# Performance work log

Hardware: AMD Instinct MI355X
Metric: run time of the kernel (lower is better)

The kernel has to match this reference:

```python
import jax, jax.numpy as jnp
import numpy as np

N, F, S, D = 8, 16, 196, 1024
H = 8
HD = D // H
L = 1 + F * S  # global feature token + f*s patch tokens


def _ln(x, g, b, eps=1e-5):
    m = x.mean(-1, keepdims=True)
    v = ((x - m) ** 2).mean(-1, keepdims=True)
    return (x - m) / jnp.sqrt(v + eps) * g + b


def _attn(q, k, v, hd):
    s = jnp.einsum('bqd,bkd->bqk', q, k) / jnp.sqrt(jnp.asarray(hd, q.dtype))
    return jnp.einsum('bqk,bkd->bqd', jax.nn.softmax(s, axis=-1), v)


def setup_inputs() -> dict:
    key = jax.random.key(0)
    ks = jax.random.split(key, 8)
    sc = 0.02
    return {
        'x': jax.random.normal(ks[0], (N, L, D), jnp.float32),
        'W_in': jax.random.normal(ks[1], (D, D), jnp.float32) * sc,
        'b_in': jnp.zeros((D,), jnp.float32),
        'g_in': jnp.ones((D,), jnp.float32),
        'beta_in': jnp.zeros((D,), jnp.float32),
        'W_q': jax.random.normal(ks[2], (D, D), jnp.float32) * sc,
        'W_k': jax.random.normal(ks[3], (D, D), jnp.float32) * sc,
        'W_v': jax.random.normal(ks[4], (D, D), jnp.float32) * sc,
        'g_out': jnp.ones((D,), jnp.float32),
        'beta_out': jnp.zeros((D,), jnp.float32),
        'W_out': jax.random.normal(ks[5], (D, D), jnp.float32) * sc,
        'b_out': jnp.zeros((D,), jnp.float32),
        'att_type': 1,  # 1 == 'time', 0 == 'space' (static)
    }


def reference(x, W_in, b_in, g_in, beta_in, W_q, W_k, W_v, g_out, beta_out, W_out, b_out, att_type):
    n = x.shape[0]
    nh = n * H
    # in_fc: Linear + LayerNorm
    x = _ln(x @ W_in + b_in, g_in, beta_in)
    q, k, v = x @ W_q, x @ W_k, x @ W_v

    def split_heads(y):  # [n, L, D] -> [n*h, L, hd]
        return y.reshape(n, L, H, HD).transpose(0, 2, 1, 3).reshape(nh, L, HD)

    q, k, v = map(split_heads, (q, k, v))
    feat_q, q = q[:, :1], q[:, 1:]
    feat_k, k = k[:, :1], k[:, 1:]
    feat_v, v = v[:, :1], v[:, 1:]

    # token_att is computed in the original but never used (dead code):
    # token_att = _attn(feat_q, k, v, HD)

    if att_type == 1:  # time attention: windows of length F per spatial site
        qt = q.reshape(nh, F, S, HD).transpose(0, 2, 1, 3).reshape(nh * S, F, HD)
        kt = k.reshape(nh, F, S, HD).transpose(0, 2, 1, 3).reshape(nh * S, F, HD)
        vt = v.reshape(nh, F, S, HD).transpose(0, 2, 1, 3).reshape(nh * S, F, HD)
        fk = jnp.tile(feat_k, (S, 1, 1))  # torch .repeat(s,1,1)
        fv = jnp.tile(feat_v, (S, 1, 1))
        kk = jnp.concatenate((fk, kt), axis=1)  # [nh*s, 1+f, hd]
        vv = jnp.concatenate((fv, vt), axis=1)
        seq = _attn(qt, kk, vv, HD)  # [nh*s, f, hd]
        seq = seq.reshape(nh, S, F, HD).transpose(0, 2, 1, 3).reshape(nh, F * S, HD)
    else:  # space attention: windows of length S per frame
        qs = q.reshape(nh * F, S, HD)
        ks_ = k.reshape(nh * F, S, HD)
        vs = v.reshape(nh * F, S, HD)
        fk = jnp.tile(feat_k, (F, 1, 1))
        fv = jnp.tile(feat_v, (F, 1, 1))
        kk = jnp.concatenate((fk, ks_), axis=1)  # [nh*f, 1+s, hd]
        vv = jnp.concatenate((fv, vs), axis=1)
        seq = _attn(qs, kk, vv, HD)  # [nh*f, s, hd]
        seq = seq.reshape(nh, F * S, HD)

    out = jnp.concatenate((feat_q, seq), axis=1)  # [nh, L, hd]
    out = out.reshape(n, H, L, HD).transpose(0, 2, 1, 3).reshape(n, L, D)
    out = _ln(out, g_out, beta_out) @ W_out + b_out
    return out
```

## Files before the change

kernel.cpp:

```cpp
#include <hip/hip_runtime.h>
#include <stdint.h>

#define N_B 8
#define F_T 16
#define S_T 196
#define D_M 1024
#define H_N 8
#define HD  128
#define L_T 3137
#define M_R (N_B * L_T)
#define M_P 25216

typedef __attribute__((ext_vector_type(8))) short bf16x8;
typedef __attribute__((ext_vector_type(4))) float f32x4;

__device__ __forceinline__ float b2f(unsigned int u) {
  union { unsigned int i; float f; } x; x.i = u << 16; return x.f;
}
__device__ __forceinline__ unsigned short f2b(float f) {
  union { float f; unsigned int i; } x; x.f = f;
  unsigned int r = x.i + 0x7fffu + ((x.i >> 16) & 1u);
  return (unsigned short)(r >> 16);
}

__global__ __launch_bounds__(256) void convert_pad(const float* __restrict__ x,
                                                   unsigned short* __restrict__ xb,
                                                   int nreal) {
  int i = (blockIdx.x * 256 + threadIdx.x) * 4;
  float4 v;
  if (i < nreal) v = *(const float4*)(x + i);
  else { v.x = 0.f; v.y = 0.f; v.z = 0.f; v.w = 0.f; }
  ushort4 o;
  o.x = f2b(v.x); o.y = f2b(v.y); o.z = f2b(v.z); o.w = f2b(v.w);
  *(ushort4*)(xb + i) = o;
}

struct WP { const float* s[5]; unsigned short* d[5]; };
__global__ __launch_bounds__(256) void transpose5(WP p) {
  __shared__ float t[32][33];
  const int w = blockIdx.z;
  const float* W = p.s[w];
  unsigned short* Wt = p.d[w];
  const int tx = threadIdx.x, ty = threadIdx.y;
  const int n0 = blockIdx.x * 32, k0 = blockIdx.y * 32;
#pragma unroll
  for (int i = 0; i < 4; i++)
    t[ty + i * 8][tx] = W[(size_t)(k0 + ty + i * 8) * D_M + n0 + tx];
  __syncthreads();
#pragma unroll
  for (int i = 0; i < 4; i++)
    Wt[(size_t)(n0 + ty + i * 8) * D_M + k0 + tx] = f2b(t[tx][ty + i * 8]);
}

__device__ __forceinline__ void async16(const unsigned short* g, unsigned short* l) {
  __builtin_amdgcn_global_load_lds((const __attribute__((address_space(1))) void*)g,
                                   (__attribute__((address_space(3))) void*)l, 16, 0, 0);
}

struct Outs { void* p[3]; };

template <int MODE>
__global__ __launch_bounds__(256) void gemm_bt(const unsigned short* __restrict__ A,
                                               const unsigned short* __restrict__ Bt,
                                               const float* __restrict__ bias,
                                               Outs o, int Mreal) {
  constexpr int NCB = (MODE == 3) ? 24 : 8;
  __shared__ __align__(16) unsigned short lds[17408];
  unsigned short* As = lds;
  unsigned short* Bs = lds + 8192;
  const int tid = threadIdx.x;
  const int lane = tid & 63;
  const int wv = tid >> 6;
  const int wm = wv >> 1, wn = wv & 1;

  const int flat = blockIdx.y * NCB + blockIdx.x;
  int rowBase, colBase;
  if (MODE == 3) {
    const int lin = (flat & 7) * 591 + (flat >> 3);
    const int cg = lin / 1576;
    const int rem = lin - cg * 1576;
    rowBase = (rem >> 3) * 128;
    colBase = (cg * 8 + (rem & 7)) * 128;
  } else {
    const int lin = (flat & 7) * 197 + (flat >> 3);
    rowBase = (lin >> 3) * 128;
    colBase = (lin & 7) * 128;
  }

  const int srow8 = lane >> 3;
  const int gk = ((lane & 7) ^ srow8) * 8;
  const unsigned short* gA = A + (size_t)(rowBase + wv * 32 + srow8) * 1024 + gk;
  const unsigned short* gB = Bt + (size_t)(colBase + wv * 32 + srow8) * 1024 + gk;
  unsigned short* lA = As + wv * 2048 + lane * 8;
  unsigned short* lB = Bs + wv * 2048 + lane * 8;

  f32x4 acc[4][4] = {};

  const int mf = lane & 15, kg = lane >> 4;
  const int sl0 = ((kg) ^ (mf & 7)) * 8;
  const int sl1 = ((4 + kg) ^ (mf & 7)) * 8;
  const unsigned short* Ar = As + (wm * 64 + mf) * 64;
  const unsigned short* Br = Bs + (wn * 64 + mf) * 64;

  for (int kt = 0; kt < 1024; kt += 64) {
    __syncthreads();
#pragma unroll
    for (int ii = 0; ii < 4; ii++) {
      async16(gA + ii * 8 * 1024 + kt, lA + ii * 512);
      async16(gB + ii * 8 * 1024 + kt, lB + ii * 512);
    }
    __syncthreads();
    {
      bf16x8 av[4], bv[4];
#pragma unroll
      for (int i = 0; i < 4; i++) av[i] = *(const bf16x8*)(Ar + i * 1024 + sl0);
#pragma unroll
      for (int j = 0; j < 4; j++) bv[j] = *(const bf16x8*)(Br + j * 1024 + sl0);
#pragma unroll
      for (int i = 0; i < 4; i++)
#pragma unroll
        for (int j = 0; j < 4; j++)
          acc[i][j] = __builtin_amdgcn_mfma_f32_16x16x32_bf16(av[i], bv[j], acc[i][j], 0, 0, 0);
    }
    {
      bf16x8 av[4], bv[4];
#pragma unroll
      for (int i = 0; i < 4; i++) av[i] = *(const bf16x8*)(Ar + i * 1024 + sl1);
#pragma unroll
      for (int j = 0; j < 4; j++) bv[j] = *(const bf16x8*)(Br + j * 1024 + sl1);
#pragma unroll
      for (int i = 0; i < 4; i++)
#pragma unroll
        for (int j = 0; j < 4; j++)
          acc[i][j] = __builtin_amdgcn_mfma_f32_16x16x32_bf16(av[i], bv[j], acc[i][j], 0, 0, 0);
    }
  }

  __syncthreads();
  if (MODE == 2) {
    float* Cf = (float*)lds;
    float* outF = (float*)o.p[0];
#pragma unroll
    for (int p = 0; p < 2; p++) {
      if (p) __syncthreads();
      if (wm == p) {
#pragma unroll
        for (int j = 0; j < 4; j++) {
          const int col_l = wn * 64 + j * 16 + mf;
          const float bval = bias[colBase + col_l];
#pragma unroll
          for (int i = 0; i < 4; i++)
#pragma unroll
            for (int r = 0; r < 4; r++)
              Cf[(i * 16 + kg * 4 + r) * 132 + col_l] = acc[i][j][r] + bval;
        }
      }
      __syncthreads();
#pragma unroll
      for (int t = 0; t < 8; t++) {
        const int g = t * 256 + tid;
        const int row = g >> 5, ch = g & 31;
        const int grow = rowBase + p * 64 + row;
        if (grow < Mreal)
          *(float4*)(outF + (size_t)grow * 1024 + colBase + ch * 4) =
              *(const float4*)(Cf + row * 132 + ch * 4);
      }
    }
  } else {
    unsigned short* Cs = lds;
#pragma unroll
    for (int j = 0; j < 4; j++) {
      const int col_l = wn * 64 + j * 16 + mf;
      const float bval = (MODE == 1) ? bias[colBase + col_l] : 0.f;
#pragma unroll
      for (int i = 0; i < 4; i++)
#pragma unroll
        for (int r = 0; r < 4; r++)
          Cs[(wm * 64 + i * 16 + kg * 4 + r) * 136 + col_l] = f2b(acc[i][j][r] + bval);
    }
    __syncthreads();
    unsigned short* C;
    int cb;
    if (MODE == 3) { C = (unsigned short*)o.p[colBase >> 10]; cb = colBase & 1023; }
    else { C = (unsigned short*)o.p[0]; cb = colBase; }
#pragma unroll
    for (int t = 0; t < 8; t++) {
      const int g = t * 256 + tid;
      const int row = g >> 4, ch = g & 15;
      *(uint4*)(C + (size_t)(rowBase + row) * 1024 + cb + ch * 8) =
          *(const uint4*)(Cs + row * 136 + ch * 8);
    }
  }
}

__global__ __launch_bounds__(256) void ln_kernel(const unsigned short* __restrict__ src,
                                                 const unsigned short* __restrict__ src0,
                                                 const float* __restrict__ g,
                                                 const float* __restrict__ beta,
                                                 unsigned short* __restrict__ out, int Mreal) {
  const int row = blockIdx.x, tid = threadIdx.x;
  unsigned short* op = out + (size_t)row * 1024 + tid * 4;
  if (row >= Mreal) {
    ushort4 z; z.x = 0; z.y = 0; z.z = 0; z.w = 0;
    *(ushort4*)op = z;
    return;
  }
  const unsigned short* s = src;
  if (src0 != nullptr && (row % L_T) == 0) s = src0;
  const unsigned short* ip = s + (size_t)row * 1024 + tid * 4;
  uint2 raw = *(const uint2*)ip;
  float x0 = b2f(raw.x & 0xffffu), x1 = b2f(raw.x >> 16);
  float x2 = b2f(raw.y & 0xffffu), x3 = b2f(raw.y >> 16);
  float sum = x0 + x1 + x2 + x3;
  float sq = x0 * x0 + x1 * x1 + x2 * x2 + x3 * x3;
#pragma unroll
  for (int off = 32; off > 0; off >>= 1) {
    sum += __shfl_down(sum, off);
    sq += __shfl_down(sq, off);
  }
  __shared__ float red[8];
  if ((tid & 63) == 0) { red[tid >> 6] = sum; red[4 + (tid >> 6)] = sq; }
  __syncthreads();
  const float ts = red[0] + red[1] + red[2] + red[3];
  const float tq = red[4] + red[5] + red[6] + red[7];
  const float mean = ts * (1.f / 1024.f);
  const float var = tq * (1.f / 1024.f) - mean * mean;
  const float rstd = rsqrtf(var + 1e-5f);
  const float4 gv = *(const float4*)(g + tid * 4);
  const float4 bv = *(const float4*)(beta + tid * 4);
  ushort4 o;
  o.x = f2b((x0 - mean) * rstd * gv.x + bv.x);
  o.y = f2b((x1 - mean) * rstd * gv.y + bv.y);
  o.z = f2b((x2 - mean) * rstd * gv.z + bv.z);
  o.w = f2b((x3 - mean) * rstd * gv.w + bv.w);
  *(ushort4*)op = o;
}

#define ATT_T_BLOCKS (64 * 49)
__global__ __launch_bounds__(256) void attn_kernel(const unsigned short* __restrict__ q,
                                                   const unsigned short* __restrict__ k,
                                                   const unsigned short* __restrict__ v,
                                                   unsigned short* __restrict__ out,
                                                   const int* __restrict__ att_type) {
  __shared__ __align__(16) char smem[22528];
  const int tid = threadIdx.x;
  const int bid = blockIdx.x;
  const int at = att_type[0];

  if (at == 1) {
    if (bid >= ATT_T_BLOCKS) return;
    const int lane = tid & 63, wv = tid >> 6;
    const int l15 = lane & 15, kg = lane >> 4;
    const int hb = bid / 49, sb = bid - hb * 49;
    const int s = sb * 4 + wv;
    const int n = hb >> 3, h = hb & 7;
    const int fi = (hb * S_T + s) & 63;
    const size_t frow = (size_t)(fi >> 3) * L_T;
    const int fcol = (fi & 7) * HD;
    const int qbase = n * L_T + 1 + s;
    const int hcol = h * HD;

    unsigned short* Pl = (unsigned short*)(smem + wv * 5632);
    unsigned short* Vl = (unsigned short*)(smem + wv * 5632 + 1024);

    {
      const int dim0 = l15 * 8;
#pragma unroll
      for (int p = 0; p < 5; p++) {
        const int key = p * 4 + kg;
        if (key < 17) {
          const unsigned short* vp = (key == 0)
              ? (v + frow * 1024 + fcol + dim0)
              : (v + (size_t)(qbase + (key - 1) * S_T) * 1024 + hcol + dim0);
          uint4 r = *(const uint4*)vp;
          unsigned int* wp = (unsigned int*)Vl + key * 65 + l15 * 4;
          wp[0] = r.x; wp[1] = r.y; wp[2] = r.z; wp[3] = r.w;
        }
      }
    }

    bf16x8 aq[4], bk0[4], bk1[4];
    {
      const unsigned short* qp = q + (size_t)(qbase + l15 * S_T) * 1024 + hcol + kg * 8;
      const unsigned short* kp = (l15 == 0)
          ? (k + frow * 1024 + fcol + kg * 8)
          : (k + (size_t)(qbase + (l15 - 1) * S_T) * 1024 + hcol + kg * 8);
      const unsigned short* kp1 = k + (size_t)(qbase + 15 * S_T) * 1024 + hcol + kg * 8;
#pragma unroll
      for (int t = 0; t < 4; t++) {
        aq[t] = *(const bf16x8*)(qp + t * 32);
        bk0[t] = *(const bf16x8*)(kp + t * 32);
        if (l15 == 0) bk1[t] = *(const bf16x8*)(kp1 + t * 32);
        else {
          bf16x8 z = {};
          bk1[t] = z;
        }
      }
    }

    f32x4 c0 = {}, c1 = {};
#pragma unroll
    for (int t = 0; t < 4; t++) {
      c0 = __builtin_amdgcn_mfma_f32_16x16x32_bf16(aq[t], bk0[t], c0, 0, 0, 0);
      c1 = __builtin_amdgcn_mfma_f32_16x16x32_bf16(aq[t], bk1[t], c1, 0, 0, 0);
    }

    const float scl = 0.08838834764831845f;
#pragma unroll
    for (int r = 0; r < 4; r++) {
      float v0 = c0[r] * scl;
      float k16 = __shfl(c1[r] * scl, lane & 48);
      float mx = v0;
#pragma unroll
      for (int m = 1; m < 16; m <<= 1) mx = fmaxf(mx, __shfl_xor(mx, m));
      mx = fmaxf(mx, k16);
      float p = __expf(v0 - mx);
      float p16 = __expf(k16 - mx);
      float sum = p;
#pragma unroll
      for (int m = 1; m < 16; m <<= 1) sum += __shfl_xor(sum, m);
      sum += p16;
      const float inv = 1.f / sum;
      const int row = kg * 4 + r;
      Pl[row * 32 + l15] = f2b(p * inv);
      Pl[row * 32 + 16 + l15] = (l15 == 0) ? f2b(p16 * inv) : (unsigned short)0;
    }

    bf16x8 ap = *(const bf16x8*)(Pl + l15 * 32 + kg * 8);
#pragma unroll
    for (int nt = 0; nt < 8; nt++) {
      const int dim = nt * 16 + l15;
      bf16x8 bv;
#pragma unroll
      for (int j = 0; j < 8; j++) {
        const int key = kg * 8 + j;
        const int kc = (key < 17) ? key : 0;
        unsigned short raw = Vl[kc * 130 + dim];
        bv[j] = (key < 17) ? (short)raw : (short)0;
      }
      f32x4 z = {};
      f32x4 o = __builtin_amdgcn_mfma_f32_16x16x32_bf16(ap, bv, z, 0, 0, 0);
#pragma unroll
      for (int r = 0; r < 4; r++) {
        const int qi = kg * 4 + r;
        out[(size_t)(qbase + qi * S_T) * 1024 + hcol + nt * 16 + l15] = f2b(o[r]);
      }
    }
    return;
  }

  float (*qs)[132] = (float (*)[132])smem;
  float (*sc)[212] = (float (*)[212])(smem + 8448);
  const int hb = bid / 208;
  const int rem = bid - hb * 208;
  const int f = rem / 13, qc = rem - f * 13;
  const int n = hb >> 3, h = hb & 7;
  const int fi = (hb * F_T + f) & 63;
  const size_t frow = (size_t)(fi >> 3) * L_T;
  const int fcol = (fi & 7) * HD;
  const int kbase = n * L_T + 1 + f * S_T;
  const int qbase = kbase + qc * 16;
  const int nk = S_T + 1;
  const int nqv = (qc == 12) ? 4 : 16;
  const int hcol = h * HD;

  {
    const int i = tid >> 4, db = (tid & 15) * 8;
    float* dst = &qs[i][db];
    if (i < nqv) {
      const unsigned short* qp = q + (size_t)(qbase + i) * 1024 + hcol + db;
      uint4 r = *(const uint4*)qp;
      dst[0] = b2f(r.x & 0xffffu); dst[1] = b2f(r.x >> 16);
      dst[2] = b2f(r.y & 0xffffu); dst[3] = b2f(r.y >> 16);
      dst[4] = b2f(r.z & 0xffffu); dst[5] = b2f(r.z >> 16);
      dst[6] = b2f(r.w & 0xffffu); dst[7] = b2f(r.w >> 16);
    } else {
#pragma unroll
      for (int u = 0; u < 8; u++) dst[u] = 0.f;
    }
  }
  __syncthreads();

  const int nslot = 16 * nk;
  for (int slot = tid; slot < nslot; slot += 256) {
    const int i = slot / nk, j = slot - i * nk;
    const unsigned short* kp = (j == 0)
        ? (k + frow * 1024 + fcol)
        : (k + (size_t)(kbase + (j - 1)) * 1024 + hcol);
    float acc = 0.f;
#pragma unroll 4
    for (int d = 0; d < 128; d += 8) {
      uint4 r = *(const uint4*)(kp + d);
      acc += qs[i][d + 0] * b2f(r.x & 0xffffu);
      acc += qs[i][d + 1] * b2f(r.x >> 16);
      acc += qs[i][d + 2] * b2f(r.y & 0xffffu);
      acc += qs[i][d + 3] * b2f(r.y >> 16);
      acc += qs[i][d + 4] * b2f(r.z & 0xffffu);
      acc += qs[i][d + 5] * b2f(r.z >> 16);
      acc += qs[i][d + 6] * b2f(r.w & 0xffffu);
      acc += qs[i][d + 7] * b2f(r.w >> 16);
    }
    sc[i][j] = acc * 0.08838834764831845f;
  }
  __syncthreads();

  if (tid < 16) {
    const int i = tid;
    float m = -1e30f;
    for (int j = 0; j < nk; j++) m = fmaxf(m, sc[i][j]);
    float ssum = 0.f;
    for (int j = 0; j < nk; j++) {
      float e = __expf(sc[i][j] - m);
      sc[i][j] = e;
      ssum += e;
    }
    const float inv = 1.f / ssum;
    for (int j = 0; j < nk; j++) sc[i][j] *= inv;
  }
  __syncthreads();

  {
    const int i = tid >> 4, db = (tid & 15) * 8;
    float o[8];
#pragma unroll
    for (int u = 0; u < 8; u++) o[u] = 0.f;
    for (int j = 0; j < nk; j++) {
      const unsigned short* vp = (j == 0)
          ? (v + frow * 1024 + fcol + db)
          : (v + (size_t)(kbase + (j - 1)) * 1024 + hcol + db);
      const float p = sc[i][j];
      uint4 r = *(const uint4*)vp;
      o[0] += p * b2f(r.x & 0xffffu); o[1] += p * b2f(r.x >> 16);
      o[2] += p * b2f(r.y & 0xffffu); o[3] += p * b2f(r.y >> 16);
      o[4] += p * b2f(r.z & 0xffffu); o[5] += p * b2f(r.z >> 16);
      o[6] += p * b2f(r.w & 0xffffu); o[7] += p * b2f(r.w >> 16);
    }
    if (i < nqv) {
      unsigned short* op = out + (size_t)(qbase + i) * 1024 + hcol + db;
      uint4 w;
      w.x = (unsigned)f2b(o[0]) | ((unsigned)f2b(o[1]) << 16);
      w.y = (unsigned)f2b(o[2]) | ((unsigned)f2b(o[3]) << 16);
      w.z = (unsigned)f2b(o[4]) | ((unsigned)f2b(o[5]) << 16);
      w.w = (unsigned)f2b(o[6]) | ((unsigned)f2b(o[7]) << 16);
      *(uint4*)op = w;
    }
  }
}

extern "C" void kernel_launch(void* const* d_in, const int* in_sizes, int n_in,
                              void* d_out, int out_size, void* d_ws, size_t ws_size,
                              hipStream_t stream) {
  const float* x        = (const float*)d_in[0];
  const float* W_in     = (const float*)d_in[1];
  const float* b_in     = (const float*)d_in[2];
  const float* g_in     = (const float*)d_in[3];
  const float* beta_in  = (const float*)d_in[4];
  const float* W_q      = (const float*)d_in[5];
  const float* W_k      = (const float*)d_in[6];
  const float* W_v      = (const float*)d_in[7];
  const float* g_out    = (const float*)d_in[8];
  const float* beta_out = (const float*)d_in[9];
  const float* W_out    = (const float*)d_in[10];
  const float* b_out    = (const float*)d_in[11];
  const int* att_type   = (const int*)d_in[12];
  float* out = (float*)d_out;

  char* ws = (char*)d_ws;
  const size_t MB = (size_t)M_P * 1024 * 2;
  unsigned short* xb = (unsigned short*)(ws + 0 * MB);
  unsigned short* t1 = (unsigned short*)(ws + 1 * MB);
  unsigned short* xh = (unsigned short*)(ws + 2 * MB);
  unsigned short* kb = (unsigned short*)(ws + 3 * MB);
  unsigned short* vb = (unsigned short*)(ws + 4 * MB);
  unsigned short* wt = (unsigned short*)(ws + 5 * MB);
  const size_t WSZ = (size_t)1024 * 1024;
  unsigned short* wt_in  = wt;
  unsigned short* wqkv   = wt + 1 * WSZ;
  unsigned short* wt_out = wt + 4 * WSZ;

  convert_pad<<<M_P, 256, 0, stream>>>(x, xb, M_R * 1024);

  WP wp;
  wp.s[0] = W_in; wp.s[1] = W_q; wp.s[2] = W_k; wp.s[3] = W_v; wp.s[4] = W_out;
  wp.d[0] = wt_in;
  wp.d[1] = wqkv;
  wp.d[2] = wqkv + 1 * WSZ;
  wp.d[3] = wqkv + 2 * WSZ;
  wp.d[4] = wt_out;
  transpose5<<<dim3(32, 32, 5), dim3(32, 8), 0, stream>>>(wp);

  Outs o1; o1.p[0] = t1; o1.p[1] = nullptr; o1.p[2] = nullptr;
  gemm_bt<1><<<dim3(8, 197), 256, 0, stream>>>(xb, wt_in, b_in, o1, M_P);
  ln_kernel<<<M_P, 256, 0, stream>>>(t1, nullptr, g_in, beta_in, xh, M_R);

  Outs oq; oq.p[0] = t1; oq.p[1] = kb; oq.p[2] = vb;
  gemm_bt<3><<<dim3(24, 197), 256, 0, stream>>>(xh, wqkv, nullptr, oq, M_P);

  attn_kernel<<<13312, 256, 0, stream>>>(t1, kb, vb, xb, att_type);
  ln_kernel<<<M_P, 256, 0, stream>>>(xb, t1, g_out, beta_out, xh, M_R);

  Outs oo; oo.p[0] = out; oo.p[1] = nullptr; oo.p[2] = nullptr;
  gemm_bt<2><<<dim3(8, 197), 256, 0, stream>>>(xh, wt_out, b_out, oo, M_R);
}
```

Before: 612.5 us.

## Rewrite GEMM as 256x256 double-buffered pipelined tile with 8 waves

Replaces the 128x128 single-buffered GEMM with a 256x256 tile per 512-thread workgroup. It double-buffers A and B in 128KB of LDS, issues async global-to-LDS loads for the next K-tile interleaved with the MFMA blocks, and raises MFMA issue priority with s_setprio. The workgroup-to-tile mapping is reordered so consecutive tiles stay on the same XCD. This is meant to hide global load latency behind compute and raise arithmetic intensity. In exchange it fills LDS, which limits occupancy, and relies on hand-placed waitcnt and barrier sequencing that is easy to get wrong.

```diff
diff --git a/kernel.cpp b/kernel.cpp
--- a/kernel.cpp
+++ b/kernel.cpp
@@ -59,136 +59,177 @@
 
 struct Outs { void* p[3]; };
 
+#define MFMA_Q(AV, MLO)                                                        \
+  __builtin_amdgcn_s_setprio(1);                                               \
+  _Pragma("unroll") for (int m_ = 0; m_ < 4; ++m_)                             \
+      _Pragma("unroll") for (int n_ = 0; n_ < 4; ++n_)                         \
+          acc[(MLO) + m_][n_] = __builtin_amdgcn_mfma_f32_16x16x32_bf16(       \
+              AV[(MLO) + m_], bv[n_], acc[(MLO) + m_][n_], 0, 0, 0);           \
+  __builtin_amdgcn_s_setprio(0);
+
+#define TILE_ONE(T, BUF, STGB, STGA, VMN)                                      \
+  do {                                                                         \
+    const unsigned short* Ab = sA + (BUF) * 16384 + aOff;                      \
+    const unsigned short* Bb = sB + (BUF) * 16384 + bOff;                      \
+    if (STGB) {                                                                \
+      async16(gB + ((T) + 1) * 64,          sBst + (1 - (BUF)) * 16384);       \
+      async16(gB + ((T) + 1) * 64 + 65536,  sBst + (1 - (BUF)) * 16384 + 4096);\
+    }                                                                          \
+    _Pragma("unroll") for (int m_ = 0; m_ < 4; ++m_)                           \
+        av0[m_] = *(const bf16x8*)(Ab + m_ * 1024 + sl0);                      \
+    _Pragma("unroll") for (int n_ = 0; n_ < 4; ++n_)                           \
+        bv[n_] = *(const bf16x8*)(Bb + n_ * 1024 + sl0);                       \
+    _Pragma("unroll") for (int m_ = 0; m_ < 4; ++m_)                           \
+        av1[m_] = *(const bf16x8*)(Ab + m_ * 1024 + sl1);                      \
+    MFMA_Q(av0, 0)                                                             \
+    if (STGB) {                                                                \
+      async16(gB + ((T) + 1) * 64 + 131072, sBst + (1 - (BUF)) * 16384 + 8192);\
+      async16(gB + ((T) + 1) * 64 + 196608, sBst + (1 - (BUF)) * 16384 + 12288);\
+    }                                                                          \
+    _Pragma("unroll") for (int m_ = 0; m_ < 4; ++m_)                           \
+        av0[4 + m_] = *(const bf16x8*)(Ab + (4 + m_) * 1024 + sl0);            \
+    _Pragma("unroll") for (int m_ = 0; m_ < 4; ++m_)                           \
+        av1[4 + m_] = *(const bf16x8*)(Ab + (4 + m_) * 1024 + sl1);            \
+    MFMA_Q(av0, 4)                                                             \
+    asm volatile("s_waitcnt lgkmcnt(0)" ::: "memory");                         \
+    __builtin_amdgcn_s_barrier();                                              \
+    asm volatile("" ::: "memory");                                             \
+    if (STGA) {                                                                \
+      async16(gA + ((T) + 2) * 64,          sAst + (BUF) * 16384);             \
+      async16(gA + ((T) + 2) * 64 + 65536,  sAst + (BUF) * 16384 + 4096);      \
+    }                                                                          \
+    _Pragma("unroll") for (int n_ = 0; n_ < 4; ++n_)                           \
+        bv[n_] = *(const bf16x8*)(Bb + n_ * 1024 + sl1);                       \
+    MFMA_Q(av1, 0)                                                             \
+    if (STGA) {                                                                \
+      async16(gA + ((T) + 2) * 64 + 131072, sAst + (BUF) * 16384 + 8192);      \
+      async16(gA + ((T) + 2) * 64 + 196608, sAst + (BUF) * 16384 + 12288);     \
+    }                                                                          \
+    MFMA_Q(av1, 4)                                                             \
+    if ((VMN) == 4)                                                            \
+      asm volatile("s_waitcnt vmcnt(4) lgkmcnt(0)" ::: "memory");              \
+    else if ((VMN) == 0)                                                       \
+      asm volatile("s_waitcnt vmcnt(0) lgkmcnt(0)" ::: "memory");              \
+    else                                                                       \
+      asm volatile("s_waitcnt lgkmcnt(0)" ::: "memory");                       \
+    __builtin_amdgcn_s_barrier();                                              \
+    asm volatile("" ::: "memory");                                             \
+  } while (0)
+
 template <int MODE>
-__global__ __launch_bounds__(256) void gemm_bt(const unsigned short* __restrict__ A,
-                                               const unsigned short* __restrict__ Bt,
-                                               const float* __restrict__ bias,
-                                               Outs o, int Mreal) {
-  constexpr int NCB = (MODE == 3) ? 24 : 8;
-  __shared__ __align__(16) unsigned short lds[17408];
-  unsigned short* As = lds;
-  unsigned short* Bs = lds + 8192;
+__global__ __launch_bounds__(512, 2) void gemm_bt(const unsigned short* __restrict__ A,
+                                                  const unsigned short* __restrict__ Bt,
+                                                  const float* __restrict__ bias,
+                                                  Outs o, int Mreal) {
+  __shared__ __align__(16) unsigned short lds[65536];
+  unsigned short* sA = lds;
+  unsigned short* sB = lds + 32768;
+
   const int tid = threadIdx.x;
   const int lane = tid & 63;
   const int wv = tid >> 6;
-  const int wm = wv >> 1, wn = wv & 1;
-
-  const int flat = blockIdx.y * NCB + blockIdx.x;
-  int rowBase, colBase;
-  if (MODE == 3) {
-    const int lin = (flat & 7) * 591 + (flat >> 3);
-    const int cg = lin / 1576;
-    const int rem = lin - cg * 1576;
-    rowBase = (rem >> 3) * 128;
-    colBase = (cg * 8 + (rem & 7)) * 128;
-  } else {
-    const int lin = (flat & 7) * 197 + (flat >> 3);
-    rowBase = (lin >> 3) * 128;
-    colBase = (lin & 7) * 128;
-  }
-
-  const int srow8 = lane >> 3;
-  const int gk = ((lane & 7) ^ srow8) * 8;
-  const unsigned short* gA = A + (size_t)(rowBase + wv * 32 + srow8) * 1024 + gk;
-  const unsigned short* gB = Bt + (size_t)(colBase + wv * 32 + srow8) * 1024 + gk;
-  unsigned short* lA = As + wv * 2048 + lane * 8;
-  unsigned short* lB = Bs + wv * 2048 + lane * 8;
-
-  f32x4 acc[4][4] = {};
-
-  const int mf = lane & 15, kg = lane >> 4;
-  const int sl0 = ((kg) ^ (mf & 7)) * 8;
-  const int sl1 = ((4 + kg) ^ (mf & 7)) * 8;
-  const unsigned short* Ar = As + (wm * 64 + mf) * 64;
-  const unsigned short* Br = Bs + (wn * 64 + mf) * 64;
-
-  for (int kt = 0; kt < 1024; kt += 64) {
-    __syncthreads();
-#pragma unroll
-    for (int ii = 0; ii < 4; ii++) {
-      async16(gA + ii * 8 * 1024 + kt, lA + ii * 512);
-      async16(gB + ii * 8 * 1024 + kt, lB + ii * 512);
-    }
-    __syncthreads();
-    {
-      bf16x8 av[4], bv[4];
-#pragma unroll
-      for (int i = 0; i < 4; i++) av[i] = *(const bf16x8*)(Ar + i * 1024 + sl0);
-#pragma unroll
-      for (int j = 0; j < 4; j++) bv[j] = *(const bf16x8*)(Br + j * 1024 + sl0);
-#pragma unroll
-      for (int i = 0; i < 4; i++)
-#pragma unroll
-        for (int j = 0; j < 4; j++)
-          acc[i][j] = __builtin_amdgcn_mfma_f32_16x16x32_bf16(av[i], bv[j], acc[i][j], 0, 0, 0);
-    }
-    {
-      bf16x8 av[4], bv[4];
-#pragma unroll
-      for (int i = 0; i < 4; i++) av[i] = *(const bf16x8*)(Ar + i * 1024 + sl1);
-#pragma unroll
-      for (int j = 0; j < 4; j++) bv[j] = *(const bf16x8*)(Br + j * 1024 + sl1);
-#pragma unroll
-      for (int i = 0; i < 4; i++)
-#pragma unroll
-        for (int j = 0; j < 4; j++)
-          acc[i][j] = __builtin_amdgcn_mfma_f32_16x16x32_bf16(av[i], bv[j], acc[i][j], 0, 0, 0);
-    }
-  }
+  const int wm = wv >> 2, wn = wv & 3;
+  const int l15 = lane & 15, kg = lane >> 4;
+
+  constexpr int NCT = (MODE == 3) ? 12 : 4;
+  constexpr int NWG = 99 * NCT;
+  constexpr int Q8 = NWG >> 3, R8 = NWG & 7;
+  const int xcd = blockIdx.x & 7, off = blockIdx.x >> 3;
+  const int lin = (xcd < R8 ? xcd * (Q8 + 1) : R8 * (Q8 + 1) + (xcd - R8) * Q8) + off;
+  const int band = lin / 396;
+  const int rem = lin - band * 396;
+  const int rowBase = (rem >> 2) * 256;
+  const int colBase = (band * 4 + (rem & 3)) * 256;
+
+  const int srow = lane >> 3;
+  const int gk = ((lane & 7) ^ srow) * 8;
+  const unsigned short* gA = A + (size_t)(rowBase + wv * 8 + srow) * 1024 + gk;
+  const unsigned short* gB = Bt + (size_t)(colBase + wv * 8 + srow) * 1024 + gk;
+  unsigned short* sAst = sA + wv * 512 + lane * 8;
+  unsigned short* sBst = sB + wv * 512 + lane * 8;
+
+  const int aOff = (wm * 128 + l15) * 64;
+  const int bOff = (wn * 64 + l15) * 64;
+  const int sl0 = ((kg) ^ (l15 & 7)) * 8;
+  const int sl1 = ((4 + kg) ^ (l15 & 7)) * 8;
+
+  f32x4 acc[8][4] = {};
+  bf16x8 av0[8], av1[8], bv[4];
+
+#pragma unroll
+  for (int i = 0; i < 4; i++) async16(gA + i * 65536, sAst + i * 4096);
+#pragma unroll
+  for (int i = 0; i < 4; i++) async16(gB + i * 65536, sBst + i * 4096);
+#pragma unroll
+  for (int i = 0; i < 4; i++) async16(gA + i * 65536 + 64, sAst + 16384 + i * 4096);
+  asm volatile("s_waitcnt vmcnt(4)" ::: "memory");
+  __builtin_amdgcn_s_barrier();
+  asm volatile("" ::: "memory");
+
+#pragma unroll 1
+  for (int tp = 0; tp < 7; ++tp) {
+    const int t0 = tp * 2;
+    TILE_ONE(t0, 0, true, true, 4);
+    TILE_ONE(t0 + 1, 1, true, true, 4);
+  }
+  TILE_ONE(14, 0, true, false, 0);
+  TILE_ONE(15, 1, false, false, -1);
 
   __syncthreads();
   if (MODE == 2) {
     float* Cf = (float*)lds;
     float* outF = (float*)o.p[0];
 #pragma unroll
-    for (int p = 0; p < 2; p++) {
+    for (int p = 0; p < 2; ++p) {
       if (p) __syncthreads();
       if (wm == p) {
 #pragma unroll
-        for (int j = 0; j < 4; j++) {
-          const int col_l = wn * 64 + j * 16 + mf;
-          const float bval = bias[colBase + col_l];
-#pragma unroll
-          for (int i = 0; i < 4; i++)
-#pragma unroll
-            for (int r = 0; r < 4; r++)
-              Cf[(i * 16 + kg * 4 + r) * 132 + col_l] = acc[i][j][r] + bval;
+        for (int n = 0; n < 4; ++n) {
+          const int col = wn * 64 + n * 16 + l15;
+          const float bval = bias[colBase + col];
+#pragma unroll
+          for (int m = 0; m < 8; ++m)
+#pragma unroll
+            for (int r = 0; r < 4; ++r)
+              Cf[(m * 16 + kg * 4 + r) * 256 + col] = acc[m][n][r] + bval;
         }
       }
       __syncthreads();
 #pragma unroll
-      for (int t = 0; t < 8; t++) {
-        const int g = t * 256 + tid;
-        const int row = g >> 5, ch = g & 31;
-        const int grow = rowBase + p * 64 + row;
+      for (int t2 = 0; t2 < 16; ++t2) {
+        const int g = t2 * 512 + tid;
+        const int row = g >> 6, ch = g & 63;
+        const int grow = rowBase + p * 128 + row;
         if (grow < Mreal)
           *(float4*)(outF + (size_t)grow * 1024 + colBase + ch * 4) =
-              *(const float4*)(Cf + row * 132 + ch * 4);
+              *(const float4*)(Cf + row * 256 + ch * 4);
       }
     }
   } else {
     unsigned short* Cs = lds;
 #pragma unroll
-    for (int j = 0; j < 4; j++) {
-      const int col_l = wn * 64 + j * 16 + mf;
-      const float bval = (MODE == 1) ? bias[colBase + col_l] : 0.f;
-#pragma unroll
-      for (int i = 0; i < 4; i++)
-#pragma unroll
-        for (int r = 0; r < 4; r++)
-          Cs[(wm * 64 + i * 16 + kg * 4 + r) * 136 + col_l] = f2b(acc[i][j][r] + bval);
+    for (int n = 0; n < 4; ++n) {
+      const int col = wn * 64 + n * 16 + l15;
+      const float bval = (MODE == 1) ? bias[colBase + col] : 0.f;
+#pragma unroll
+      for (int m = 0; m < 8; ++m)
+#pragma unroll
+        for (int r = 0; r < 4; ++r)
+          Cs[(wm * 128 + m * 16 + kg * 4 + r) * 256 + col] = f2b(acc[m][n][r] + bval);
     }
     __syncthreads();
     unsigned short* C;
-    int cb;
-    if (MODE == 3) { C = (unsigned short*)o.p[colBase >> 10]; cb = colBase & 1023; }
-    else { C = (unsigned short*)o.p[0]; cb = colBase; }
-#pragma unroll
-    for (int t = 0; t < 8; t++) {
-      const int g = t * 256 + tid;
-      const int row = g >> 4, ch = g & 15;
-      *(uint4*)(C + (size_t)(rowBase + row) * 1024 + cb + ch * 8) =
-          *(const uint4*)(Cs + row * 136 + ch * 8);
+    int cbase;
+    if (MODE == 3) { C = (unsigned short*)o.p[colBase >> 10]; cbase = colBase & 1023; }
+    else { C = (unsigned short*)o.p[0]; cbase = colBase; }
+#pragma unroll
+    for (int t2 = 0; t2 < 16; ++t2) {
+      const int g = t2 * 512 + tid;
+      const int row = g >> 5, ch = g & 31;
+      const int grow = rowBase + row;
+      if (grow < Mreal)
+        *(uint4*)(C + (size_t)grow * 1024 + cbase + ch * 8) =
+            *(const uint4*)(Cs + row * 256 + ch * 8);
     }
   }
 }
@@ -330,16 +371,16 @@
 #pragma unroll
     for (int nt = 0; nt < 8; nt++) {
       const int dim = nt * 16 + l15;
-      bf16x8 bv;
+      bf16x8 bvv;
 #pragma unroll
       for (int j = 0; j < 8; j++) {
         const int key = kg * 8 + j;
         const int kc = (key < 17) ? key : 0;
         unsigned short raw = Vl[kc * 130 + dim];
-        bv[j] = (key < 17) ? (short)raw : (short)0;
+        bvv[j] = (key < 17) ? (short)raw : (short)0;
       }
       f32x4 z = {};
-      f32x4 o = __builtin_amdgcn_mfma_f32_16x16x32_bf16(ap, bv, z, 0, 0, 0);
+      f32x4 o = __builtin_amdgcn_mfma_f32_16x16x32_bf16(ap, bvv, z, 0, 0, 0);
 #pragma unroll
       for (int r = 0; r < 4; r++) {
         const int qi = kg * 4 + r;
@@ -490,15 +531,15 @@
   transpose5<<<dim3(32, 32, 5), dim3(32, 8), 0, stream>>>(wp);
 
   Outs o1; o1.p[0] = t1; o1.p[1] = nullptr; o1.p[2] = nullptr;
-  gemm_bt<1><<<dim3(8, 197), 256, 0, stream>>>(xb, wt_in, b_in, o1, M_P);
+  gemm_bt<1><<<396, 512, 0, stream>>>(xb, wt_in, b_in, o1, M_P);
   ln_kernel<<<M_P, 256, 0, stream>>>(t1, nullptr, g_in, beta_in, xh, M_R);
 
   Outs oq; oq.p[0] = t1; oq.p[1] = kb; oq.p[2] = vb;
-  gemm_bt<3><<<dim3(24, 197), 256, 0, stream>>>(xh, wqkv, nullptr, oq, M_P);
+  gemm_bt<3><<<1188, 512, 0, stream>>>(xh, wqkv, nullptr, oq, M_P);
 
   attn_kernel<<<13312, 256, 0, stream>>>(t1, kb, vb, xb, att_type);
   ln_kernel<<<M_P, 256, 0, stream>>>(xb, t1, g_out, beta_out, xh, M_R);
 
   Outs oo; oo.p[0] = out; oo.p[1] = nullptr; oo.p[2] = nullptr;
-  gemm_bt<2><<<dim3(8, 197), 256, 0, stream>>>(xh, wt_out, b_out, oo, M_R);
-}
+  gemm_bt<2><<<396, 512, 0, stream>>>(xh, wt_out, b_out, oo, M_R);
+}
```

New measurement: 539.1 us. -12.0%, faster.
